# Kernel optimization log

Measured on AMD Instinct MI355X. Metric: run time of the kernel, lower is better.

The kernel has to match this reference:

```python
import jax, jax.numpy as jnp
import numpy as np

N = 100_000   # nodes
E = 1_600_000 # edges (avg degree 16)
D = 128       # numeric_dim
H = 128       # hidden_dim
C = 2         # num_classes
EPS = 1e-5    # BatchNorm eps


def setup_inputs() -> dict:
    key = jax.random.key(0)
    ks = jax.random.split(key, 24)

    def lin(k, i, o):  # torch Linear init-ish, stored as [in, out]
        return (jax.random.normal(k, (i, o), jnp.float32) / np.sqrt(i)).astype(jnp.float32)

    inp = {
        "x": jax.random.normal(ks[0], (N, D), jnp.float32),
        "edge_index": jax.random.randint(ks[1], (2, E), 0, N),
        "in_w": lin(ks[2], D, H),
        "in_b": jnp.zeros((H,), jnp.float32),
        "cls_w": lin(ks[3], H, C),
        "cls_b": jnp.zeros((C,), jnp.float32),
    }
    k = 4
    for blk in ("b1", "b2", "b3"):
        inp[f"{blk}_lw"] = lin(ks[k + 0], H, H)      # SAGEConv lin_l (aggregated neighbors), has bias
        inp[f"{blk}_lb"] = jnp.zeros((H,), jnp.float32)
        inp[f"{blk}_rw"] = lin(ks[k + 1], H, H)      # SAGEConv lin_r (root), bias=False in PyG
        inp[f"{blk}_g"] = jnp.ones((H,), jnp.float32)   # BN gamma
        inp[f"{blk}_bt"] = jnp.zeros((H,), jnp.float32)  # BN beta
        k += 2
    return inp


def _sage_block(x, src, dst, lw, lb, rw, g, bt):
    # SAGEConv with mean aggregation: messages flow src -> dst
    agg = jax.ops.segment_sum(x[src], dst, num_segments=N)            # [N, H]
    deg = jax.ops.segment_sum(jnp.ones((src.shape[0], 1), x.dtype), dst, num_segments=N)
    mean = agg / jnp.maximum(deg, 1.0)
    out = mean @ lw + lb + x @ rw                                     # lin_l(mean) + lin_r(x)
    # BatchNorm1d (training-mode batch stats over nodes), biased variance
    mu = out.mean(axis=0)
    var = out.var(axis=0)
    out = (out - mu) * jax.lax.rsqrt(var + EPS) * g + bt
    out = jax.nn.relu(out)
    # dropout in eval mode = identity; skip is Identity (H == H)
    return out + x


def reference(x, edge_index, in_w, in_b, cls_w, cls_b,
              b1_lw, b1_lb, b1_rw, b1_g, b1_bt,
              b2_lw, b2_lb, b2_rw, b2_g, b2_bt,
              b3_lw, b3_lb, b3_rw, b3_g, b3_bt):
    src, dst = edge_index[0], edge_index[1]
    h = jax.nn.relu(x @ in_w + in_b)
    h = _sage_block(h, src, dst, b1_lw, b1_lb, b1_rw, b1_g, b1_bt)
    h = _sage_block(h, src, dst, b2_lw, b2_lb, b2_rw, b2_g, b2_bt)
    h = _sage_block(h, src, dst, b3_lw, b3_lb, b3_rw, b3_g, b3_bt)
    return h @ cls_w + cls_b  # [N, C] logits
```

## Files before the change

### kernel.cpp

```cpp
#include <hip/hip_runtime.h>

#define NN 100000
#define NE 1600000
#define HD 128
#define EPSI 1e-5f

using u32 = unsigned int;
using u16 = unsigned short;
using u64 = unsigned long long;

typedef short bf16x8 __attribute__((ext_vector_type(8)));
typedef float f32x4  __attribute__((ext_vector_type(4)));

constexpr int SCAN_CHUNK  = 1024;
constexpr int SCAN_BLOCKS = (NN + SCAN_CHUNK - 1) / SCAN_CHUNK;
constexpr int NRANGE      = 128;
constexpr int RSZ2        = 784;
constexpr int BINCAP      = 16384;
constexpr int PART_CHUNK4 = 1024;
constexpr int PART_GRID   = (NE / 4 + PART_CHUNK4 - 1) / PART_CHUNK4;

__device__ inline float bflo(u32 u) { return __uint_as_float(u << 16); }
__device__ inline float bfhi(u32 u) { return __uint_as_float(u & 0xFFFF0000u); }
__device__ inline u16 f2bf(float f) {
    u32 u = __float_as_uint(f);
    u += 0x7FFFu + ((u >> 16) & 1u);
    return (u16)(u >> 16);
}
__device__ inline u32 pack2(float a, float b) {
    return (u32)f2bf(a) | ((u32)f2bf(b) << 16);
}


__global__ __launch_bounds__(256) void k_part(const int* __restrict__ src,
                                              const int* __restrict__ dst,
                                              int* __restrict__ binCur,
                                              u64* __restrict__ binbuf) {
    __shared__ int hist[NRANGE], base[NRANGE], curs[NRANGE];
    const int t  = threadIdx.x;
    const int c0 = blockIdx.x * PART_CHUNK4;
    if (t < NRANGE) { hist[t] = 0; curs[t] = 0; }
    __syncthreads();

    int4 ds[4], ss[4];
    bool ok[4];
#pragma unroll
    for (int i = 0; i < 4; ++i) {
        const int c = c0 + t + 256 * i;
        ok[i] = c < NE / 4;
        if (ok[i]) {
            ds[i] = reinterpret_cast<const int4*>(dst)[c];
            ss[i] = reinterpret_cast<const int4*>(src)[c];
        }
    }
#pragma unroll
    for (int i = 0; i < 4; ++i) {
        if (ok[i]) {
            atomicAdd(&hist[ds[i].x / RSZ2], 1);
            atomicAdd(&hist[ds[i].y / RSZ2], 1);
            atomicAdd(&hist[ds[i].z / RSZ2], 1);
            atomicAdd(&hist[ds[i].w / RSZ2], 1);
        }
    }
    __syncthreads();
    if (t < NRANGE && hist[t] > 0) base[t] = atomicAdd(&binCur[t], hist[t]);
    __syncthreads();

#pragma unroll
    for (int i = 0; i < 4; ++i) {
        if (ok[i]) {
            const int d[4] = {ds[i].x, ds[i].y, ds[i].z, ds[i].w};
            const int s[4] = {ss[i].x, ss[i].y, ss[i].z, ss[i].w};
#pragma unroll
            for (int j = 0; j < 4; ++j) {
                const int r = d[j] / RSZ2;
                const int p = base[r] + atomicAdd(&curs[r], 1);
                if (p < BINCAP)
                    binbuf[(size_t)r * BINCAP + p] = ((u64)(u32)s[j] << 32) | (u32)d[j];
            }
        }
    }
}

__global__ __launch_bounds__(1024) void k_countL(const int* __restrict__ binCur,
                                                 const u64* __restrict__ binbuf,
                                                 int* __restrict__ cnt) {
    __shared__ int hist[RSZ2];
    const int b = blockIdx.x;
    const int t = threadIdx.x;
    for (int i = t; i < RSZ2; i += 1024) hist[i] = 0;
    __syncthreads();
    const int n = min(binCur[b], BINCAP);
    const u64* bin = binbuf + (size_t)b * BINCAP;
    for (int i = t; i < n; i += 1024)
        atomicAdd(&hist[(int)(u32)(bin[i] & 0xFFFFFFFFu) - b * RSZ2], 1);
    __syncthreads();
    for (int i = t; i < RSZ2; i += 1024) {
        const int idx = b * RSZ2 + i;
        if (idx < NN) cnt[idx] = hist[i];
    }
}

__global__ void k_scan1(const int* __restrict__ cnt, int* __restrict__ rp,
                        int* __restrict__ tot) {
    __shared__ int lds[256];
    const int t    = threadIdx.x;
    const int base = blockIdx.x * SCAN_CHUNK + t * 4;
    int v[4];
#pragma unroll
    for (int i = 0; i < 4; ++i) v[i] = (base + i < NN) ? cnt[base + i] : 0;
    const int s = v[0] + v[1] + v[2] + v[3];
    lds[t] = s;
    __syncthreads();
    int val = s;
    for (int off = 1; off < 256; off <<= 1) {
        int other = (t >= off) ? lds[t - off] : 0;
        __syncthreads();
        val += other;
        lds[t] = val;
        __syncthreads();
    }
    int e = val - s;
#pragma unroll
    for (int i = 0; i < 4; ++i) {
        if (base + i < NN) rp[base + i] = e;
        e += v[i];
    }
    if (t == 255) tot[blockIdx.x] = val;
}

__global__ void k_scan2(int* __restrict__ tot, int* __restrict__ rp) {
    __shared__ int l[128];
    const int t = threadIdx.x;
    const int v = (t < SCAN_BLOCKS) ? tot[t] : 0;
    l[t] = v;
    __syncthreads();
    int val = v;
    for (int off = 1; off < 128; off <<= 1) {
        const int o = (t >= off) ? l[t - off] : 0;
        __syncthreads();
        val += o;
        l[t] = val;
        __syncthreads();
    }
    if (t < SCAN_BLOCKS) tot[t] = val - v;
    if (t == 127) rp[NN] = val;
}

__global__ void k_scan3(int* __restrict__ rp, const int* __restrict__ tot) {
    int idx = blockIdx.x * 256 + threadIdx.x;
    if (idx < NN) rp[idx] += tot[idx >> 10];
}

__global__ __launch_bounds__(1024) void k_fillL(const int* __restrict__ binCur,
                                                const u64* __restrict__ binbuf,
                                                const int* __restrict__ rp,
                                                int* __restrict__ col) {
    __shared__ int cur[RSZ2];
    const int b = blockIdx.x;
    const int t = threadIdx.x;
    for (int i = t; i < RSZ2; i += 1024) {
        const int idx = b * RSZ2 + i;
        cur[i] = (idx < NN) ? rp[idx] : 0;
    }
    __syncthreads();
    const int n = min(binCur[b], BINCAP);
    const u64* bin = binbuf + (size_t)b * BINCAP;
    for (int i = t; i < n; i += 1024) {
        const u64 e = bin[i];
        const int d = (int)(u32)(e & 0xFFFFFFFFu);
        const int s = (int)(u32)(e >> 32);
        col[atomicAdd(&cur[d - b * RSZ2], 1)] = s;
    }
}


struct WTArgs { const float* w[7]; u16* o[7]; };

__global__ void k_wt(WTArgs a) {
    const int m = blockIdx.y;
    const int n = blockIdx.x;
    const int k = threadIdx.x;
    a.o[m][n * HD + k] = f2bf(a.w[m][k * HD + n]);
}


__device__ inline void acc8(float* a, uint4 v) {
    a[0] += bflo(v.x); a[1] += bfhi(v.x);
    a[2] += bflo(v.y); a[3] += bfhi(v.y);
    a[4] += bflo(v.z); a[5] += bfhi(v.z);
    a[6] += bflo(v.w); a[7] += bfhi(v.w);
}

__global__ __launch_bounds__(256) void k_agg(const u16* __restrict__ h,
                                             const int* __restrict__ rp,
                                             const int* __restrict__ col,
                                             u16* __restrict__ mean) {
    const int lane = threadIdx.x & 63;
    const int node = blockIdx.x * 4 + (threadIdx.x >> 6);
    const int grp  = lane >> 4;
    const int li   = lane & 15;
    const int r0 = rp[node], r1 = rp[node + 1];
    const size_t lof = (size_t)li * 8;
    float a[8];
#pragma unroll
    for (int i = 0; i < 8; ++i) a[i] = 0.f;
    int e = r0 + grp;
    for (; e + 12 < r1; e += 16) {
        const int s0 = col[e], s1 = col[e + 4], s2 = col[e + 8], s3 = col[e + 12];
        const uint4 v0 = *reinterpret_cast<const uint4*>(&h[(size_t)s0 * HD + lof]);
        const uint4 v1 = *reinterpret_cast<const uint4*>(&h[(size_t)s1 * HD + lof]);
        const uint4 v2 = *reinterpret_cast<const uint4*>(&h[(size_t)s2 * HD + lof]);
        const uint4 v3 = *reinterpret_cast<const uint4*>(&h[(size_t)s3 * HD + lof]);
        acc8(a, v0); acc8(a, v1); acc8(a, v2); acc8(a, v3);
    }
    for (; e < r1; e += 4) {
        const uint4 v = *reinterpret_cast<const uint4*>(&h[(size_t)col[e] * HD + lof]);
        acc8(a, v);
    }
#pragma unroll
    for (int i = 0; i < 8; ++i) {
        a[i] += __shfl_xor(a[i], 16);
        a[i] += __shfl_xor(a[i], 32);
    }
    if (lane < 16) {
        const float inv = 1.0f / fmaxf((float)(r1 - r0), 1.0f);
        uint4 o;
        o.x = pack2(a[0] * inv, a[1] * inv);
        o.y = pack2(a[2] * inv, a[3] * inv);
        o.z = pack2(a[4] * inv, a[5] * inv);
        o.w = pack2(a[6] * inv, a[7] * inv);
        *reinterpret_cast<uint4*>(&mean[(size_t)node * HD + lof]) = o;
    }
}


template <int A1F32, int RELU, int STATS>
__global__ __launch_bounds__(256) void k_mgemm(
    const void* __restrict__ A1p, const u16* __restrict__ W1T,
    const u16* __restrict__ A2, const u16* __restrict__ W2T,
    const float* __restrict__ bias, u16* __restrict__ out,
    float* __restrict__ stats)
{
    __shared__ uint4 Wlds[2048];
    const int t    = threadIdx.x;
    const int wv   = t >> 6;
    const int lane = t & 63;
    const int lid  = lane & 15;
    const int kseg = lane >> 4;
    const int row0 = blockIdx.x * 128 + wv * 32;

    f32x4 acc[2][8];
#pragma unroll
    for (int rf = 0; rf < 2; ++rf)
#pragma unroll
        for (int c = 0; c < 8; ++c) acc[rf][c] = (f32x4){0.f, 0.f, 0.f, 0.f};

    int  ar[2];
    bool rok[2];
#pragma unroll
    for (int rf = 0; rf < 2; ++rf) {
        ar[rf]  = row0 + rf * 16 + lid;
        rok[rf] = ar[rf] < NN;
    }

    for (int pass = 0; pass < 2; ++pass) {
        if (pass == 1 && A2 == nullptr) break;
        const u16* WT = pass ? W2T : W1T;
        if (pass) __syncthreads();
#pragma unroll
        for (int i = 0; i < 8; ++i) {
            const int g   = t + 256 * i;
            const int row = g >> 4;
            const int ch  = g & 15;
            Wlds[row * 16 + (ch ^ (row & 7))] = reinterpret_cast<const uint4*>(WT)[g];
        }
        bf16x8 af[2][4];
        if (A1F32 && pass == 0) {
            const float* A = (const float*)A1p;
#pragma unroll
            for (int rf = 0; rf < 2; ++rf)
#pragma unroll
                for (int kk = 0; kk < 4; ++kk) {
                    const int kof = kk * 32 + kseg * 8;
                    if (rok[rf]) {
                        const float4 f0 = *reinterpret_cast<const float4*>(&A[(size_t)ar[rf] * HD + kof]);
                        const float4 f1 = *reinterpret_cast<const float4*>(&A[(size_t)ar[rf] * HD + kof + 4]);
                        af[rf][kk][0] = (short)f2bf(f0.x); af[rf][kk][1] = (short)f2bf(f0.y);
                        af[rf][kk][2] = (short)f2bf(f0.z); af[rf][kk][3] = (short)f2bf(f0.w);
                        af[rf][kk][4] = (short)f2bf(f1.x); af[rf][kk][5] = (short)f2bf(f1.y);
                        af[rf][kk][6] = (short)f2bf(f1.z); af[rf][kk][7] = (short)f2bf(f1.w);
                    } else {
                        af[rf][kk] = (bf16x8)0;
                    }
                }
        } else {
            const u16* A = pass ? A2 : (const u16*)A1p;
#pragma unroll
            for (int rf = 0; rf < 2; ++rf)
#pragma unroll
                for (int kk = 0; kk < 4; ++kk) {
                    const int kof = kk * 32 + kseg * 8;
                    af[rf][kk] = rok[rf]
                        ? *reinterpret_cast<const bf16x8*>(&A[(size_t)ar[rf] * HD + kof])
                        : (bf16x8)0;
                }
        }
        __syncthreads();
#pragma unroll
        for (int kk = 0; kk < 4; ++kk) {
#pragma unroll
            for (int c = 0; c < 8; ++c) {
                const int brow = c * 16 + lid;
                const bf16x8 bf = *reinterpret_cast<const bf16x8*>(
                    &Wlds[brow * 16 + ((kk * 4 + kseg) ^ (lid & 7))]);
#pragma unroll
                for (int rf = 0; rf < 2; ++rf)
                    acc[rf][c] = __builtin_amdgcn_mfma_f32_16x16x32_bf16(af[rf][kk], bf, acc[rf][c], 0, 0, 0);
            }
        }
    }

    float bv[8];
#pragma unroll
    for (int c = 0; c < 8; ++c) bv[c] = bias[c * 16 + lid];

    float sv[8], qv[8];
#pragma unroll
    for (int c = 0; c < 8; ++c) { sv[c] = 0.f; qv[c] = 0.f; }

#pragma unroll
    for (int rf = 0; rf < 2; ++rf) {
#pragma unroll
        for (int c = 0; c < 8; ++c) {
            const int colc = c * 16 + lid;
#pragma unroll
            for (int j = 0; j < 4; ++j) {
                const int rrow = row0 + rf * 16 + kseg * 4 + j;
                if (rrow < NN) {
                    float o = acc[rf][c][j] + bv[c];
                    if (RELU) o = fmaxf(o, 0.f);
                    out[(size_t)rrow * HD + colc] = f2bf(o);
                    sv[c] += o;
                    qv[c] += o * o;
                }
            }
        }
    }

    if constexpr (STATS) {
        __shared__ float ls[4][HD], lq[4][HD];
#pragma unroll
        for (int c = 0; c < 8; ++c) {
            sv[c] += __shfl_xor(sv[c], 16);
            sv[c] += __shfl_xor(sv[c], 32);
            qv[c] += __shfl_xor(qv[c], 16);
            qv[c] += __shfl_xor(qv[c], 32);
        }
        if (lane < 16) {
#pragma unroll
            for (int c = 0; c < 8; ++c) {
                ls[wv][c * 16 + lid] = sv[c];
                lq[wv][c * 16 + lid] = qv[c];
            }
        }
        __syncthreads();
        if (t < HD) {
            const float s = (ls[0][t] + ls[1][t]) + (ls[2][t] + ls[3][t]);
            atomicAdd(&stats[t], s);
        } else {
            const int j = t - HD;
            const float q = (lq[0][j] + lq[1][j]) + (lq[2][j] + lq[3][j]);
            atomicAdd(&stats[HD + j], q);
        }
    }
}


template <int CLS>
__global__ __launch_bounds__(256) void k_apply(
    const u16* __restrict__ outb, const float* __restrict__ stats,
    const float* __restrict__ g, const float* __restrict__ bt,
    u16* __restrict__ hb, const float* __restrict__ cw,
    const float* __restrict__ cb, float* __restrict__ logits)
{
    const int t = threadIdx.x;
    const size_t idx4 = (size_t)blockIdx.x * 256 + t;
    const int j = (int)(idx4 & 31) * 4;
    const float4 svv = *reinterpret_cast<const float4*>(&stats[j]);
    const float4 qvv = *reinterpret_cast<const float4*>(&stats[HD + j]);
    const float4 gv  = *reinterpret_cast<const float4*>(&g[j]);
    const float4 bv  = *reinterpret_cast<const float4*>(&bt[j]);
    const float invn = 1.0f / (float)NN;
    float sc[4], sh[4];
    {
        const float sa[4] = {svv.x, svv.y, svv.z, svv.w};
        const float qa[4] = {qvv.x, qvv.y, qvv.z, qvv.w};
        const float ga[4] = {gv.x, gv.y, gv.z, gv.w};
        const float ba[4] = {bv.x, bv.y, bv.z, bv.w};
#pragma unroll
        for (int i = 0; i < 4; ++i) {
            const float mean = sa[i] * invn;
            const float var  = qa[i] * invn - mean * mean;
            sc[i] = ga[i] * rsqrtf(var + EPSI);
            sh[i] = ba[i] - mean * sc[i];
        }
    }
    const uint2 o  = reinterpret_cast<const uint2*>(outb)[idx4];
    const uint2 hv = reinterpret_cast<const uint2*>(hb)[idx4];
    const float r0 = fmaxf(bflo(o.x) * sc[0] + sh[0], 0.f) + bflo(hv.x);
    const float r1 = fmaxf(bfhi(o.x) * sc[1] + sh[1], 0.f) + bfhi(hv.x);
    const float r2 = fmaxf(bflo(o.y) * sc[2] + sh[2], 0.f) + bflo(hv.y);
    const float r3 = fmaxf(bfhi(o.y) * sc[3] + sh[3], 0.f) + bfhi(hv.y);
    reinterpret_cast<uint2*>(hb)[idx4] = make_uint2(pack2(r0, r1), pack2(r2, r3));

    if constexpr (CLS) {
        const float4 w01 = *reinterpret_cast<const float4*>(&cw[j * 2]);
        const float4 w23 = *reinterpret_cast<const float4*>(&cw[j * 2 + 4]);
        float p0 = r0 * w01.x + r1 * w01.z + r2 * w23.x + r3 * w23.z;
        float p1 = r0 * w01.y + r1 * w01.w + r2 * w23.y + r3 * w23.w;
#pragma unroll
        for (int off = 1; off <= 16; off <<= 1) {
            p0 += __shfl_xor(p0, off);
            p1 += __shfl_xor(p1, off);
        }
        if ((t & 31) == 0) {
            const size_t row = idx4 >> 5;
            logits[row * 2 + 0] = p0 + cb[0];
            logits[row * 2 + 1] = p1 + cb[1];
        }
    }
}


extern "C" void kernel_launch(void* const* d_in, const int* in_sizes, int n_in,
                              void* d_out, int out_size, void* d_ws, size_t ws_size,
                              hipStream_t stream) {
    const float* x     = (const float*)d_in[0];
    const int*   ei    = (const int*)d_in[1];
    const float* in_w  = (const float*)d_in[2];
    const float* in_b  = (const float*)d_in[3];
    const float* cls_w = (const float*)d_in[4];
    const float* cls_b = (const float*)d_in[5];
    const float* blk_w[3][5];
    for (int bidx = 0; bidx < 3; ++bidx)
        for (int k = 0; k < 5; ++k)
            blk_w[bidx][k] = (const float*)d_in[6 + bidx * 5 + k];

    const int* src = ei;
    const int* dst = ei + NE;

    size_t off = 0;
    auto alloc = [&](size_t bytes) {
        void* p = (char*)d_ws + off;
        off += (bytes + 255) & ~(size_t)255;
        return p;
    };
    u16*   h      = (u16*)alloc((size_t)NN * HD * 2);
    u16*   tmp    = (u16*)alloc((size_t)NN * HD * 2);
    int*   rp     = (int*)alloc((size_t)(NN + 1) * 4);
    int*   cnt    = (int*)alloc((size_t)NN * 4);
    int*   col    = (int*)alloc((size_t)NE * 4);
    int*   stot   = (int*)alloc((size_t)SCAN_BLOCKS * 4);
    u16*   wtb    = (u16*)alloc((size_t)7 * HD * HD * 2);
    const size_t off_z = off;
    float* stats  = (float*)alloc((size_t)3 * 256 * 4);
    int*   binCur = (int*)alloc((size_t)NRANGE * 4);
    const size_t zspan = off - off_z;
    u64*   binbuf = (u64*)tmp;
    (void)ws_size; (void)n_in; (void)in_sizes; (void)out_size;

    hipMemsetAsync(stats, 0, zspan, stream);

    WTArgs wa;
    wa.w[0] = in_w;
    for (int bidx = 0; bidx < 3; ++bidx) {
        wa.w[1 + bidx * 2] = blk_w[bidx][0];
        wa.w[2 + bidx * 2] = blk_w[bidx][2];
    }
    for (int m = 0; m < 7; ++m) wa.o[m] = wtb + (size_t)m * HD * HD;
    k_wt<<<dim3(HD, 7), HD, 0, stream>>>(wa);

    k_part<<<PART_GRID, 256, 0, stream>>>(src, dst, binCur, binbuf);
    k_countL<<<NRANGE, 1024, 0, stream>>>(binCur, binbuf, cnt);
    k_scan1<<<SCAN_BLOCKS, 256, 0, stream>>>(cnt, rp, stot);
    k_scan2<<<1, 128, 0, stream>>>(stot, rp);
    k_scan3<<<(NN + 255) / 256, 256, 0, stream>>>(rp, stot);
    k_fillL<<<NRANGE, 1024, 0, stream>>>(binCur, binbuf, rp, col);

    const int gemm_grid  = (NN + 127) / 128;
    const int apply_grid = NN * 32 / 256;

    k_mgemm<1, 1, 0><<<gemm_grid, 256, 0, stream>>>(x, wtb, nullptr, nullptr, in_b, h, nullptr);

    for (int bidx = 0; bidx < 3; ++bidx) {
        const u16* lwT = wtb + (size_t)(1 + bidx * 2) * HD * HD;
        const u16* rwT = wtb + (size_t)(2 + bidx * 2) * HD * HD;
        const float* lb = blk_w[bidx][1];
        const float* g  = blk_w[bidx][3];
        const float* bt = blk_w[bidx][4];
        float* st = stats + bidx * 256;
        k_agg<<<NN / 4, 256, 0, stream>>>(h, rp, col, tmp);
        k_mgemm<0, 0, 1><<<gemm_grid, 256, 0, stream>>>(tmp, lwT, h, rwT, lb, tmp, st);
        if (bidx < 2)
            k_apply<0><<<apply_grid, 256, 0, stream>>>(tmp, st, g, bt, h,
                                                       nullptr, nullptr, nullptr);
        else
            k_apply<1><<<apply_grid, 256, 0, stream>>>(tmp, st, g, bt, h,
                                                       cls_w, cls_b, (float*)d_out);
    }
}
```

Before: 404.9 us.

## Switch node features to chunk-major layout and one-thread-per-node aggregation

```diff
diff --git a/kernel.cpp b/kernel.cpp
--- a/kernel.cpp
+++ b/kernel.cpp
@@ -7,10 +7,10 @@
 
 using u32 = unsigned int;
 using u16 = unsigned short;
-using u64 = unsigned long long;
 
 typedef short bf16x8 __attribute__((ext_vector_type(8)));
 typedef float f32x4  __attribute__((ext_vector_type(4)));
+typedef u32   u32x4  __attribute__((ext_vector_type(4)));
 
 constexpr int SCAN_CHUNK  = 1024;
 constexpr int SCAN_BLOCKS = (NN + SCAN_CHUNK - 1) / SCAN_CHUNK;
@@ -20,6 +20,7 @@
 constexpr int PART_CHUNK4 = 1024;
 constexpr int PART_GRID   = (NE / 4 + PART_CHUNK4 - 1) / PART_CHUNK4;
 
+
 __device__ inline float bflo(u32 u) { return __uint_as_float(u << 16); }
 __device__ inline float bfhi(u32 u) { return __uint_as_float(u & 0xFFFF0000u); }
 __device__ inline u16 f2bf(float f) {
@@ -35,7 +36,7 @@
 __global__ __launch_bounds__(256) void k_part(const int* __restrict__ src,
                                               const int* __restrict__ dst,
                                               int* __restrict__ binCur,
-                                              u64* __restrict__ binbuf) {
+                                              u32* __restrict__ binbuf) {
     __shared__ int hist[NRANGE], base[NRANGE], curs[NRANGE];
     const int t  = threadIdx.x;
     const int c0 = blockIdx.x * PART_CHUNK4;
@@ -73,17 +74,18 @@
             const int s[4] = {ss[i].x, ss[i].y, ss[i].z, ss[i].w};
 #pragma unroll
             for (int j = 0; j < 4; ++j) {
-                const int r = d[j] / RSZ2;
-                const int p = base[r] + atomicAdd(&curs[r], 1);
+                const int r  = d[j] / RSZ2;
+                const int ld = d[j] - r * RSZ2;
+                const int p  = base[r] + atomicAdd(&curs[r], 1);
                 if (p < BINCAP)
-                    binbuf[(size_t)r * BINCAP + p] = ((u64)(u32)s[j] << 32) | (u32)d[j];
+                    binbuf[(size_t)r * BINCAP + p] = ((u32)s[j] << 10) | (u32)ld;
             }
         }
     }
 }
 
 __global__ __launch_bounds__(1024) void k_countL(const int* __restrict__ binCur,
-                                                 const u64* __restrict__ binbuf,
+                                                 const u32* __restrict__ binbuf,
                                                  int* __restrict__ cnt) {
     __shared__ int hist[RSZ2];
     const int b = blockIdx.x;
@@ -91,9 +93,9 @@
     for (int i = t; i < RSZ2; i += 1024) hist[i] = 0;
     __syncthreads();
     const int n = min(binCur[b], BINCAP);
-    const u64* bin = binbuf + (size_t)b * BINCAP;
+    const u32* bin = binbuf + (size_t)b * BINCAP;
     for (int i = t; i < n; i += 1024)
-        atomicAdd(&hist[(int)(u32)(bin[i] & 0xFFFFFFFFu) - b * RSZ2], 1);
+        atomicAdd(&hist[bin[i] & 1023u], 1);
     __syncthreads();
     for (int i = t; i < RSZ2; i += 1024) {
         const int idx = b * RSZ2 + i;
@@ -153,7 +155,7 @@
 }
 
 __global__ __launch_bounds__(1024) void k_fillL(const int* __restrict__ binCur,
-                                                const u64* __restrict__ binbuf,
+                                                const u32* __restrict__ binbuf,
                                                 const int* __restrict__ rp,
                                                 int* __restrict__ col) {
     __shared__ int cur[RSZ2];
@@ -165,12 +167,10 @@
     }
     __syncthreads();
     const int n = min(binCur[b], BINCAP);
-    const u64* bin = binbuf + (size_t)b * BINCAP;
+    const u32* bin = binbuf + (size_t)b * BINCAP;
     for (int i = t; i < n; i += 1024) {
-        const u64 e = bin[i];
-        const int d = (int)(u32)(e & 0xFFFFFFFFu);
-        const int s = (int)(u32)(e >> 32);
-        col[atomicAdd(&cur[d - b * RSZ2], 1)] = s;
+        const u32 e = bin[i];
+        col[atomicAdd(&cur[e & 1023u], 1)] = (int)(e >> 10);
     }
 }
 
@@ -185,7 +185,7 @@
 }
 
 
-__device__ inline void acc8(float* a, uint4 v) {
+__device__ inline void acc8(float* a, u32x4 v) {
     a[0] += bflo(v.x); a[1] += bfhi(v.x);
     a[2] += bflo(v.y); a[3] += bfhi(v.y);
     a[4] += bflo(v.z); a[5] += bfhi(v.z);
@@ -196,42 +196,31 @@
                                              const int* __restrict__ rp,
                                              const int* __restrict__ col,
                                              u16* __restrict__ mean) {
-    const int lane = threadIdx.x & 63;
-    const int node = blockIdx.x * 4 + (threadIdx.x >> 6);
-    const int grp  = lane >> 4;
-    const int li   = lane & 15;
+    const int s    = blockIdx.x & 15;
+    const int node = (blockIdx.x >> 4) * 256 + threadIdx.x;
+    if (node >= NN) return;
     const int r0 = rp[node], r1 = rp[node + 1];
-    const size_t lof = (size_t)li * 8;
+    const u32x4* hs = reinterpret_cast<const u32x4*>(h) + (size_t)s * NN;
     float a[8];
 #pragma unroll
     for (int i = 0; i < 8; ++i) a[i] = 0.f;
-    int e = r0 + grp;
-    for (; e + 12 < r1; e += 16) {
-        const int s0 = col[e], s1 = col[e + 4], s2 = col[e + 8], s3 = col[e + 12];
-        const uint4 v0 = *reinterpret_cast<const uint4*>(&h[(size_t)s0 * HD + lof]);
-        const uint4 v1 = *reinterpret_cast<const uint4*>(&h[(size_t)s1 * HD + lof]);
-        const uint4 v2 = *reinterpret_cast<const uint4*>(&h[(size_t)s2 * HD + lof]);
-        const uint4 v3 = *reinterpret_cast<const uint4*>(&h[(size_t)s3 * HD + lof]);
+    int e = r0;
+    for (; e + 4 <= r1; e += 4) {
+        const int s0 = col[e], s1 = col[e + 1], s2 = col[e + 2], s3 = col[e + 3];
+        const u32x4 v0 = hs[s0];
+        const u32x4 v1 = hs[s1];
+        const u32x4 v2 = hs[s2];
+        const u32x4 v3 = hs[s3];
         acc8(a, v0); acc8(a, v1); acc8(a, v2); acc8(a, v3);
     }
-    for (; e < r1; e += 4) {
-        const uint4 v = *reinterpret_cast<const uint4*>(&h[(size_t)col[e] * HD + lof]);
-        acc8(a, v);
-    }
-#pragma unroll
-    for (int i = 0; i < 8; ++i) {
-        a[i] += __shfl_xor(a[i], 16);
-        a[i] += __shfl_xor(a[i], 32);
-    }
-    if (lane < 16) {
-        const float inv = 1.0f / fmaxf((float)(r1 - r0), 1.0f);
-        uint4 o;
-        o.x = pack2(a[0] * inv, a[1] * inv);
-        o.y = pack2(a[2] * inv, a[3] * inv);
-        o.z = pack2(a[4] * inv, a[5] * inv);
-        o.w = pack2(a[6] * inv, a[7] * inv);
-        *reinterpret_cast<uint4*>(&mean[(size_t)node * HD + lof]) = o;
-    }
+    for (; e < r1; ++e) acc8(a, hs[col[e]]);
+    const float inv = 1.0f / fmaxf((float)(r1 - r0), 1.0f);
+    u32x4 o;
+    o.x = pack2(a[0] * inv, a[1] * inv);
+    o.y = pack2(a[2] * inv, a[3] * inv);
+    o.z = pack2(a[4] * inv, a[5] * inv);
+    o.w = pack2(a[6] * inv, a[7] * inv);
+    __builtin_nontemporal_store(o, reinterpret_cast<u32x4*>(mean) + (size_t)s * NN + node);
 }
 
 
@@ -242,7 +231,7 @@
     const float* __restrict__ bias, u16* __restrict__ out,
     float* __restrict__ stats)
 {
-    __shared__ uint4 Wlds[2048];
+    __shared__ u32x4 Wlds[2048];
     const int t    = threadIdx.x;
     const int wv   = t >> 6;
     const int lane = t & 63;
@@ -273,7 +262,7 @@
             const int g   = t + 256 * i;
             const int row = g >> 4;
             const int ch  = g & 15;
-            Wlds[row * 16 + (ch ^ (row & 7))] = reinterpret_cast<const uint4*>(WT)[g];
+            Wlds[row * 16 + (ch ^ (row & 7))] = reinterpret_cast<const u32x4*>(WT)[g];
         }
         bf16x8 af[2][4];
         if (A1F32 && pass == 0) {
@@ -300,9 +289,9 @@
             for (int rf = 0; rf < 2; ++rf)
 #pragma unroll
                 for (int kk = 0; kk < 4; ++kk) {
-                    const int kof = kk * 32 + kseg * 8;
+                    const int chunk = kk * 4 + kseg;
                     af[rf][kk] = rok[rf]
-                        ? *reinterpret_cast<const bf16x8*>(&A[(size_t)ar[rf] * HD + kof])
+                        ? *reinterpret_cast<const bf16x8*>(&A[((size_t)chunk * NN + ar[rf]) * 8])
                         : (bf16x8)0;
                 }
         }
@@ -333,14 +322,16 @@
     for (int rf = 0; rf < 2; ++rf) {
 #pragma unroll
         for (int c = 0; c < 8; ++c) {
-            const int colc = c * 16 + lid;
+            const int colc  = c * 16 + lid;
+            const int chunk = colc >> 3;
+            const int w8    = colc & 7;
 #pragma unroll
             for (int j = 0; j < 4; ++j) {
                 const int rrow = row0 + rf * 16 + kseg * 4 + j;
                 if (rrow < NN) {
                     float o = acc[rf][c][j] + bv[c];
                     if (RELU) o = fmaxf(o, 0.f);
-                    out[(size_t)rrow * HD + colc] = f2bf(o);
+                    out[((size_t)chunk * NN + rrow) * 8 + w8] = f2bf(o);
                     sv[c] += o;
                     qv[c] += o * o;
                 }
@@ -377,58 +368,61 @@
 }
 
 
-template <int CLS>
 __global__ __launch_bounds__(256) void k_apply(
     const u16* __restrict__ outb, const float* __restrict__ stats,
     const float* __restrict__ g, const float* __restrict__ bt,
-    u16* __restrict__ hb, const float* __restrict__ cw,
-    const float* __restrict__ cb, float* __restrict__ logits)
+    u16* __restrict__ hb)
 {
-    const int t = threadIdx.x;
-    const size_t idx4 = (size_t)blockIdx.x * 256 + t;
-    const int j = (int)(idx4 & 31) * 4;
-    const float4 svv = *reinterpret_cast<const float4*>(&stats[j]);
-    const float4 qvv = *reinterpret_cast<const float4*>(&stats[HD + j]);
-    const float4 gv  = *reinterpret_cast<const float4*>(&g[j]);
-    const float4 bv  = *reinterpret_cast<const float4*>(&bt[j]);
+    const int chunk = blockIdx.y;
+    const int node  = blockIdx.x * 256 + threadIdx.x;
+    if (node >= NN) return;
+    const int j0 = chunk * 8;
     const float invn = 1.0f / (float)NN;
-    float sc[4], sh[4];
-    {
-        const float sa[4] = {svv.x, svv.y, svv.z, svv.w};
-        const float qa[4] = {qvv.x, qvv.y, qvv.z, qvv.w};
-        const float ga[4] = {gv.x, gv.y, gv.z, gv.w};
-        const float ba[4] = {bv.x, bv.y, bv.z, bv.w};
-#pragma unroll
-        for (int i = 0; i < 4; ++i) {
-            const float mean = sa[i] * invn;
-            const float var  = qa[i] * invn - mean * mean;
-            sc[i] = ga[i] * rsqrtf(var + EPSI);
-            sh[i] = ba[i] - mean * sc[i];
-        }
-    }
-    const uint2 o  = reinterpret_cast<const uint2*>(outb)[idx4];
-    const uint2 hv = reinterpret_cast<const uint2*>(hb)[idx4];
-    const float r0 = fmaxf(bflo(o.x) * sc[0] + sh[0], 0.f) + bflo(hv.x);
-    const float r1 = fmaxf(bfhi(o.x) * sc[1] + sh[1], 0.f) + bfhi(hv.x);
-    const float r2 = fmaxf(bflo(o.y) * sc[2] + sh[2], 0.f) + bflo(hv.y);
-    const float r3 = fmaxf(bfhi(o.y) * sc[3] + sh[3], 0.f) + bfhi(hv.y);
-    reinterpret_cast<uint2*>(hb)[idx4] = make_uint2(pack2(r0, r1), pack2(r2, r3));
-
-    if constexpr (CLS) {
-        const float4 w01 = *reinterpret_cast<const float4*>(&cw[j * 2]);
-        const float4 w23 = *reinterpret_cast<const float4*>(&cw[j * 2 + 4]);
-        float p0 = r0 * w01.x + r1 * w01.z + r2 * w23.x + r3 * w23.z;
-        float p1 = r0 * w01.y + r1 * w01.w + r2 * w23.y + r3 * w23.w;
-#pragma unroll
-        for (int off = 1; off <= 16; off <<= 1) {
-            p0 += __shfl_xor(p0, off);
-            p1 += __shfl_xor(p1, off);
-        }
-        if ((t & 31) == 0) {
-            const size_t row = idx4 >> 5;
-            logits[row * 2 + 0] = p0 + cb[0];
-            logits[row * 2 + 1] = p1 + cb[1];
-        }
+    float sc[8], sh[8];
+#pragma unroll
+    for (int i = 0; i < 8; ++i) {
+        const float mean = stats[j0 + i] * invn;
+        const float var  = stats[HD + j0 + i] * invn - mean * mean;
+        const float s    = g[j0 + i] * rsqrtf(var + EPSI);
+        sc[i] = s;
+        sh[i] = bt[j0 + i] - mean * s;
+    }
+    const size_t idx = (size_t)chunk * NN + node;
+    const u32x4 o  = reinterpret_cast<const u32x4*>(outb)[idx];
+    const u32x4 hv = reinterpret_cast<const u32x4*>(hb)[idx];
+    const u32 ov[4] = {o.x, o.y, o.z, o.w};
+    const u32 hu[4] = {hv.x, hv.y, hv.z, hv.w};
+    u32x4 res;
+#pragma unroll
+    for (int i = 0; i < 4; ++i) {
+        const float r0 = fmaxf(bflo(ov[i]) * sc[i * 2 + 0] + sh[i * 2 + 0], 0.f) + bflo(hu[i]);
+        const float r1 = fmaxf(bfhi(ov[i]) * sc[i * 2 + 1] + sh[i * 2 + 1], 0.f) + bfhi(hu[i]);
+        res[i] = pack2(r0, r1);
+    }
+    reinterpret_cast<u32x4*>(hb)[idx] = res;
+}
+
+
+__global__ void k_cls(const u16* __restrict__ h, const float* __restrict__ w,
+                      const float* __restrict__ b, float* __restrict__ out) {
+    const int lane = threadIdx.x & 63;
+    const int i = (int)((blockIdx.x * 256 + threadIdx.x) >> 6);
+    if (i >= NN) return;
+    const int chunk = lane >> 2;
+    const int off   = (lane & 3) * 2;
+    const u32 v = *reinterpret_cast<const u32*>(&h[((size_t)chunk * NN + i) * 8 + off]);
+    const float h0 = bflo(v), h1 = bfhi(v);
+    const float4 wv = *reinterpret_cast<const float4*>(&w[lane * 4]);
+    float a0 = h0 * wv.x + h1 * wv.z;
+    float a1 = h0 * wv.y + h1 * wv.w;
+#pragma unroll
+    for (int off2 = 32; off2 > 0; off2 >>= 1) {
+        a0 += __shfl_xor(a0, off2);
+        a1 += __shfl_xor(a1, off2);
+    }
+    if (lane == 0) {
+        out[(size_t)i * 2 + 0] = a0 + b[0];
+        out[(size_t)i * 2 + 1] = a1 + b[1];
     }
 }
 
@@ -467,10 +461,10 @@
     float* stats  = (float*)alloc((size_t)3 * 256 * 4);
     int*   binCur = (int*)alloc((size_t)NRANGE * 4);
     const size_t zspan = off - off_z;
-    u64*   binbuf = (u64*)tmp;
+    u32*   binbuf = (u32*)tmp;
     (void)ws_size; (void)n_in; (void)in_sizes; (void)out_size;
 
-    hipMemsetAsync(stats, 0, zspan, stream);
+    (void)hipMemsetAsync(stats, 0, zspan, stream);
 
     WTArgs wa;
     wa.w[0] = in_w;
@@ -488,8 +482,10 @@
     k_scan3<<<(NN + 255) / 256, 256, 0, stream>>>(rp, stot);
     k_fillL<<<NRANGE, 1024, 0, stream>>>(binCur, binbuf, rp, col);
 
-    const int gemm_grid  = (NN + 127) / 128;
-    const int apply_grid = NN * 32 / 256;
+    const int  nodeb      = (NN + 255) / 256;
+    const int  gemm_grid  = (NN + 127) / 128;
+    const int  agg_grid   = nodeb * 16;
+    const dim3 apply_grid(nodeb, 16);
 
     k_mgemm<1, 1, 0><<<gemm_grid, 256, 0, stream>>>(x, wtb, nullptr, nullptr, in_b, h, nullptr);
 
@@ -500,13 +496,10 @@
         const float* g  = blk_w[bidx][3];
         const float* bt = blk_w[bidx][4];
         float* st = stats + bidx * 256;
-        k_agg<<<NN / 4, 256, 0, stream>>>(h, rp, col, tmp);
+        k_agg<<<agg_grid, 256, 0, stream>>>(h, rp, col, tmp);
         k_mgemm<0, 0, 1><<<gemm_grid, 256, 0, stream>>>(tmp, lwT, h, rwT, lb, tmp, st);
-        if (bidx < 2)
-            k_apply<0><<<apply_grid, 256, 0, stream>>>(tmp, st, g, bt, h,
-                                                       nullptr, nullptr, nullptr);
-        else
-            k_apply<1><<<apply_grid, 256, 0, stream>>>(tmp, st, g, bt, h,
-                                                       cls_w, cls_b, (float*)d_out);
-    }
-}
+        k_apply<<<apply_grid, 256, 0, stream>>>(tmp, st, g, bt, h);
+    }
+
+    k_cls<<<(NN + 3) / 4, 256, 0, stream>>>(h, cls_w, cls_b, (float*)d_out);
+}
```

New measurement: 668.3 us. 1.65x slower.

## Pack edge bins into 32-bit words and prefetch both GEMM operands up front

Applied to the files above, without the earlier changes.

```diff
diff --git a/kernel.cpp b/kernel.cpp
--- a/kernel.cpp
+++ b/kernel.cpp
@@ -7,10 +7,10 @@
 
 using u32 = unsigned int;
 using u16 = unsigned short;
-using u64 = unsigned long long;
 
 typedef short bf16x8 __attribute__((ext_vector_type(8)));
 typedef float f32x4  __attribute__((ext_vector_type(4)));
+typedef u32   u32x4  __attribute__((ext_vector_type(4)));
 
 constexpr int SCAN_CHUNK  = 1024;
 constexpr int SCAN_BLOCKS = (NN + SCAN_CHUNK - 1) / SCAN_CHUNK;
@@ -35,7 +35,7 @@
 __global__ __launch_bounds__(256) void k_part(const int* __restrict__ src,
                                               const int* __restrict__ dst,
                                               int* __restrict__ binCur,
-                                              u64* __restrict__ binbuf) {
+                                              u32* __restrict__ binbuf) {
     __shared__ int hist[NRANGE], base[NRANGE], curs[NRANGE];
     const int t  = threadIdx.x;
     const int c0 = blockIdx.x * PART_CHUNK4;
@@ -73,17 +73,18 @@
             const int s[4] = {ss[i].x, ss[i].y, ss[i].z, ss[i].w};
 #pragma unroll
             for (int j = 0; j < 4; ++j) {
-                const int r = d[j] / RSZ2;
-                const int p = base[r] + atomicAdd(&curs[r], 1);
+                const int r  = d[j] / RSZ2;
+                const int ld = d[j] - r * RSZ2;
+                const int p  = base[r] + atomicAdd(&curs[r], 1);
                 if (p < BINCAP)
-                    binbuf[(size_t)r * BINCAP + p] = ((u64)(u32)s[j] << 32) | (u32)d[j];
+                    binbuf[(size_t)r * BINCAP + p] = ((u32)s[j] << 10) | (u32)ld;
             }
         }
     }
 }
 
 __global__ __launch_bounds__(1024) void k_countL(const int* __restrict__ binCur,
-                                                 const u64* __restrict__ binbuf,
+                                                 const u32* __restrict__ binbuf,
                                                  int* __restrict__ cnt) {
     __shared__ int hist[RSZ2];
     const int b = blockIdx.x;
@@ -91,9 +92,9 @@
     for (int i = t; i < RSZ2; i += 1024) hist[i] = 0;
     __syncthreads();
     const int n = min(binCur[b], BINCAP);
-    const u64* bin = binbuf + (size_t)b * BINCAP;
+    const u32* bin = binbuf + (size_t)b * BINCAP;
     for (int i = t; i < n; i += 1024)
-        atomicAdd(&hist[(int)(u32)(bin[i] & 0xFFFFFFFFu) - b * RSZ2], 1);
+        atomicAdd(&hist[bin[i] & 1023u], 1);
     __syncthreads();
     for (int i = t; i < RSZ2; i += 1024) {
         const int idx = b * RSZ2 + i;
@@ -153,7 +154,7 @@
 }
 
 __global__ __launch_bounds__(1024) void k_fillL(const int* __restrict__ binCur,
-                                                const u64* __restrict__ binbuf,
+                                                const u32* __restrict__ binbuf,
                                                 const int* __restrict__ rp,
                                                 int* __restrict__ col) {
     __shared__ int cur[RSZ2];
@@ -165,12 +166,10 @@
     }
     __syncthreads();
     const int n = min(binCur[b], BINCAP);
-    const u64* bin = binbuf + (size_t)b * BINCAP;
+    const u32* bin = binbuf + (size_t)b * BINCAP;
     for (int i = t; i < n; i += 1024) {
-        const u64 e = bin[i];
-        const int d = (int)(u32)(e & 0xFFFFFFFFu);
-        const int s = (int)(u32)(e >> 32);
-        col[atomicAdd(&cur[d - b * RSZ2], 1)] = s;
+        const u32 e = bin[i];
+        col[atomicAdd(&cur[e & 1023u], 1)] = (int)(e >> 10);
     }
 }
 
@@ -185,7 +184,7 @@
 }
 
 
-__device__ inline void acc8(float* a, uint4 v) {
+__device__ inline void acc8(float* a, u32x4 v) {
     a[0] += bflo(v.x); a[1] += bfhi(v.x);
     a[2] += bflo(v.y); a[3] += bfhi(v.y);
     a[4] += bflo(v.z); a[5] += bfhi(v.z);
@@ -208,14 +207,14 @@
     int e = r0 + grp;
     for (; e + 12 < r1; e += 16) {
         const int s0 = col[e], s1 = col[e + 4], s2 = col[e + 8], s3 = col[e + 12];
-        const uint4 v0 = *reinterpret_cast<const uint4*>(&h[(size_t)s0 * HD + lof]);
-        const uint4 v1 = *reinterpret_cast<const uint4*>(&h[(size_t)s1 * HD + lof]);
-        const uint4 v2 = *reinterpret_cast<const uint4*>(&h[(size_t)s2 * HD + lof]);
-        const uint4 v3 = *reinterpret_cast<const uint4*>(&h[(size_t)s3 * HD + lof]);
+        const u32x4 v0 = *reinterpret_cast<const u32x4*>(&h[(size_t)s0 * HD + lof]);
+        const u32x4 v1 = *reinterpret_cast<const u32x4*>(&h[(size_t)s1 * HD + lof]);
+        const u32x4 v2 = *reinterpret_cast<const u32x4*>(&h[(size_t)s2 * HD + lof]);
+        const u32x4 v3 = *reinterpret_cast<const u32x4*>(&h[(size_t)s3 * HD + lof]);
         acc8(a, v0); acc8(a, v1); acc8(a, v2); acc8(a, v3);
     }
     for (; e < r1; e += 4) {
-        const uint4 v = *reinterpret_cast<const uint4*>(&h[(size_t)col[e] * HD + lof]);
+        const u32x4 v = *reinterpret_cast<const u32x4*>(&h[(size_t)col[e] * HD + lof]);
         acc8(a, v);
     }
 #pragma unroll
@@ -225,12 +224,12 @@
     }
     if (lane < 16) {
         const float inv = 1.0f / fmaxf((float)(r1 - r0), 1.0f);
-        uint4 o;
+        u32x4 o;
         o.x = pack2(a[0] * inv, a[1] * inv);
         o.y = pack2(a[2] * inv, a[3] * inv);
         o.z = pack2(a[4] * inv, a[5] * inv);
         o.w = pack2(a[6] * inv, a[7] * inv);
-        *reinterpret_cast<uint4*>(&mean[(size_t)node * HD + lof]) = o;
+        *reinterpret_cast<u32x4*>(&mean[(size_t)node * HD + lof]) = o;
     }
 }
 
@@ -242,7 +241,7 @@
     const float* __restrict__ bias, u16* __restrict__ out,
     float* __restrict__ stats)
 {
-    __shared__ uint4 Wlds[2048];
+    __shared__ u32x4 Wlds[2048];
     const int t    = threadIdx.x;
     const int wv   = t >> 6;
     const int lane = t & 63;
@@ -264,47 +263,85 @@
         rok[rf] = ar[rf] < NN;
     }
 
-    for (int pass = 0; pass < 2; ++pass) {
-        if (pass == 1 && A2 == nullptr) break;
-        const u16* WT = pass ? W2T : W1T;
-        if (pass) __syncthreads();
+#pragma unroll
+    for (int i = 0; i < 8; ++i) {
+        const int g   = t + 256 * i;
+        const int row = g >> 4;
+        const int ch  = g & 15;
+        Wlds[row * 16 + (ch ^ (row & 7))] = reinterpret_cast<const u32x4*>(W1T)[g];
+    }
+    u32x4 wreg[8];
+    if (A2 != nullptr) {
+#pragma unroll
+        for (int i = 0; i < 8; ++i)
+            wreg[i] = reinterpret_cast<const u32x4*>(W2T)[t + 256 * i];
+    }
+
+    bf16x8 af1[2][4], af2[2][4];
+    if (A1F32) {
+        const float* A = (const float*)A1p;
+#pragma unroll
+        for (int rf = 0; rf < 2; ++rf)
+#pragma unroll
+            for (int kk = 0; kk < 4; ++kk) {
+                const int kof = kk * 32 + kseg * 8;
+                if (rok[rf]) {
+                    const float4 f0 = *reinterpret_cast<const float4*>(&A[(size_t)ar[rf] * HD + kof]);
+                    const float4 f1 = *reinterpret_cast<const float4*>(&A[(size_t)ar[rf] * HD + kof + 4]);
+                    af1[rf][kk][0] = (short)f2bf(f0.x); af1[rf][kk][1] = (short)f2bf(f0.y);
+                    af1[rf][kk][2] = (short)f2bf(f0.z); af1[rf][kk][3] = (short)f2bf(f0.w);
+                    af1[rf][kk][4] = (short)f2bf(f1.x); af1[rf][kk][5] = (short)f2bf(f1.y);
+                    af1[rf][kk][6] = (short)f2bf(f1.z); af1[rf][kk][7] = (short)f2bf(f1.w);
+                } else {
+                    af1[rf][kk] = (bf16x8)0;
+                }
+            }
+    } else {
+        const u16* A = (const u16*)A1p;
+#pragma unroll
+        for (int rf = 0; rf < 2; ++rf)
+#pragma unroll
+            for (int kk = 0; kk < 4; ++kk) {
+                const int kof = kk * 32 + kseg * 8;
+                af1[rf][kk] = rok[rf]
+                    ? *reinterpret_cast<const bf16x8*>(&A[(size_t)ar[rf] * HD + kof])
+                    : (bf16x8)0;
+            }
+    }
+    if (A2 != nullptr) {
+#pragma unroll
+        for (int rf = 0; rf < 2; ++rf)
+#pragma unroll
+            for (int kk = 0; kk < 4; ++kk) {
+                const int kof = kk * 32 + kseg * 8;
+                af2[rf][kk] = rok[rf]
+                    ? *reinterpret_cast<const bf16x8*>(&A2[(size_t)ar[rf] * HD + kof])
+                    : (bf16x8)0;
+            }
+    }
+
+    __syncthreads();
+#pragma unroll
+    for (int kk = 0; kk < 4; ++kk) {
+#pragma unroll
+        for (int c = 0; c < 8; ++c) {
+            const int brow = c * 16 + lid;
+            const bf16x8 bf = *reinterpret_cast<const bf16x8*>(
+                &Wlds[brow * 16 + ((kk * 4 + kseg) ^ (lid & 7))]);
+#pragma unroll
+            for (int rf = 0; rf < 2; ++rf)
+                acc[rf][c] = __builtin_amdgcn_mfma_f32_16x16x32_bf16(af1[rf][kk], bf, acc[rf][c], 0, 0, 0);
+        }
+    }
+
+    if (A2 != nullptr) {
+        __syncthreads();
 #pragma unroll
         for (int i = 0; i < 8; ++i) {
             const int g   = t + 256 * i;
             const int row = g >> 4;
             const int ch  = g & 15;
-            Wlds[row * 16 + (ch ^ (row & 7))] = reinterpret_cast<const uint4*>(WT)[g];
-        }
-        bf16x8 af[2][4];
-        if (A1F32 && pass == 0) {
-            const float* A = (const float*)A1p;
-#pragma unroll
-            for (int rf = 0; rf < 2; ++rf)
-#pragma unroll
-                for (int kk = 0; kk < 4; ++kk) {
-                    const int kof = kk * 32 + kseg * 8;
-                    if (rok[rf]) {
-                        const float4 f0 = *reinterpret_cast<const float4*>(&A[(size_t)ar[rf] * HD + kof]);
-                        const float4 f1 = *reinterpret_cast<const float4*>(&A[(size_t)ar[rf] * HD + kof + 4]);
-                        af[rf][kk][0] = (short)f2bf(f0.x); af[rf][kk][1] = (short)f2bf(f0.y);
-                        af[rf][kk][2] = (short)f2bf(f0.z); af[rf][kk][3] = (short)f2bf(f0.w);
-                        af[rf][kk][4] = (short)f2bf(f1.x); af[rf][kk][5] = (short)f2bf(f1.y);
-                        af[rf][kk][6] = (short)f2bf(f1.z); af[rf][kk][7] = (short)f2bf(f1.w);
-                    } else {
-                        af[rf][kk] = (bf16x8)0;
-                    }
-                }
-        } else {
-            const u16* A = pass ? A2 : (const u16*)A1p;
-#pragma unroll
-            for (int rf = 0; rf < 2; ++rf)
-#pragma unroll
-                for (int kk = 0; kk < 4; ++kk) {
-                    const int kof = kk * 32 + kseg * 8;
-                    af[rf][kk] = rok[rf]
-                        ? *reinterpret_cast<const bf16x8*>(&A[(size_t)ar[rf] * HD + kof])
-                        : (bf16x8)0;
-                }
+            Wlds[row * 16 + (ch ^ (row & 7))] = wreg[i];
         }
         __syncthreads();
 #pragma unroll
@@ -316,7 +353,7 @@
                     &Wlds[brow * 16 + ((kk * 4 + kseg) ^ (lid & 7))]);
 #pragma unroll
                 for (int rf = 0; rf < 2; ++rf)
-                    acc[rf][c] = __builtin_amdgcn_mfma_f32_16x16x32_bf16(af[rf][kk], bf, acc[rf][c], 0, 0, 0);
+                    acc[rf][c] = __builtin_amdgcn_mfma_f32_16x16x32_bf16(af2[rf][kk], bf, acc[rf][c], 0, 0, 0);
             }
         }
     }
@@ -467,10 +504,10 @@
     float* stats  = (float*)alloc((size_t)3 * 256 * 4);
     int*   binCur = (int*)alloc((size_t)NRANGE * 4);
     const size_t zspan = off - off_z;
-    u64*   binbuf = (u64*)tmp;
+    u32*   binbuf = (u32*)tmp;
     (void)ws_size; (void)n_in; (void)in_sizes; (void)out_size;
 
-    hipMemsetAsync(stats, 0, zspan, stream);
+    (void)hipMemsetAsync(stats, 0, zspan, stream);
 
     WTArgs wa;
     wa.w[0] = in_w;
```

New measurement: 397.3 us. No clear change (-1.9%).
